# Kernel optimization log

Measured on AMD Instinct MI355X. Metric: run time of the kernel, lower is better.

Reference implementation:

```python
import jax, jax.numpy as jnp
import numpy as np

NUM_TEAMS = 100000
INPUT_SIZE = 128
HIDDEN = 128
NUM_MATCHES = 1000000
OUT = 3


def setup_inputs() -> dict:
    key = jax.random.key(0)
    ks = jax.random.split(key, 10)
    s_ih = 1.0 / np.sqrt(HIDDEN)
    inputs = jax.random.normal(ks[0], (NUM_TEAMS, INPUT_SIZE), dtype=jnp.float32)
    hx = jax.random.normal(ks[1], (NUM_TEAMS, HIDDEN), dtype=jnp.float32)
    cx = jax.random.normal(ks[2], (NUM_TEAMS, HIDDEN), dtype=jnp.float32)
    matches = jax.random.randint(ks[3], (NUM_MATCHES, 2), 0, NUM_TEAMS, dtype=jnp.int64)
    W_ih = jax.random.uniform(ks[4], (4 * HIDDEN, INPUT_SIZE), jnp.float32, -s_ih, s_ih)
    W_hh = jax.random.uniform(ks[5], (4 * HIDDEN, HIDDEN), jnp.float32, -s_ih, s_ih)
    b_ih = jax.random.uniform(ks[6], (4 * HIDDEN,), jnp.float32, -s_ih, s_ih)
    b_hh = jax.random.uniform(ks[7], (4 * HIDDEN,), jnp.float32, -s_ih, s_ih)
    s_o = 1.0 / np.sqrt(2 * HIDDEN)
    W_out = jax.random.uniform(ks[8], (OUT, 2 * HIDDEN), jnp.float32, -s_o, s_o)
    b_out = jax.random.uniform(ks[9], (OUT,), jnp.float32, -s_o, s_o)
    return {"inputs": inputs, "hx": hx, "cx": cx, "matches": matches,
            "W_ih": W_ih, "W_hh": W_hh, "b_ih": b_ih, "b_hh": b_hh,
            "W_out": W_out, "b_out": b_out}


def reference(inputs, hx, cx, matches, W_ih, W_hh, b_ih, b_hh, W_out, b_out):
    # Batched LSTMCell step across all teams (replaces per-team Python loop).
    gates = inputs @ W_ih.T + b_ih + hx @ W_hh.T + b_hh  # [T, 4H]
    i_g, f_g, g_g, o_g = jnp.split(gates, 4, axis=1)
    c_new = jax.nn.sigmoid(f_g) * cx + jax.nn.sigmoid(i_g) * jnp.tanh(g_g)
    h_new = jax.nn.sigmoid(o_g) * jnp.tanh(c_new)  # [T, H]
    # Fused gather + concat + linear + softmax for all matches.
    home = h_new[matches[:, 0]]  # [M, H]
    away = h_new[matches[:, 1]]  # [M, H]
    feat = jnp.concatenate([home, away], axis=1)  # [M, 2H]
    logits = feat @ W_out.T + b_out  # [M, 3]
    pmf = jax.nn.softmax(logits, axis=-1)
    return pmf
```

## Files before the change

### kernel.cpp

```cpp
#include <hip/hip_runtime.h>
#include <hip/hip_bf16.h>

typedef __bf16 bf16x8 __attribute__((ext_vector_type(8)));
typedef float f32x4 __attribute__((ext_vector_type(4)));

#define NUM_TEAMS 100000
#define NUM_MATCHES 1000000
#define LOG2E 1.4426950408889634f
#define NWG 3126
#define XQ 390
#define XR 6

__device__ __forceinline__ unsigned short f2bf(float x) {
    __hip_bfloat16 h = __float2bfloat16(x);
    return reinterpret_cast<unsigned short&>(h);
}
__device__ __forceinline__ unsigned int cvtpk(float a, float b) {
    unsigned int r;
    asm("v_cvt_pk_bf16_f32 %0, %1, %2" : "=v"(r) : "v"(a), "v"(b));
    return r;
}
__device__ __forceinline__ float exp2_(float x) {
    float r; asm("v_exp_f32 %0, %1" : "=v"(r) : "v"(x)); return r;
}
__device__ __forceinline__ float rcp_(float x) {
    float r; asm("v_rcp_f32 %0, %1" : "=v"(r) : "v"(x)); return r;
}

__global__ __launch_bounds__(256) void prep_kernel(
    const float* __restrict__ W_ih, const float* __restrict__ W_hh,
    const float* __restrict__ b_ih, const float* __restrict__ b_hh,
    unsigned short* __restrict__ Wpk, float* __restrict__ biasc)
{
    int gid = blockIdx.x * 256 + threadIdx.x;
    int e = gid & 7;
    int chunk = gid >> 3;
    int l15 = chunk & 15;
    int l4 = (chunk >> 4) & 3;
    int rest = chunk >> 6;
    int ks = rest & 7;
    int gate = (rest >> 3) & 3;
    int G = rest >> 5;
    int row = gate * 128 + G * 16 + l15;
    int k = ks * 32 + l4 * 8 + e;
    float v = (k < 128) ? W_ih[row * 128 + k] : W_hh[row * 128 + (k - 128)];
    Wpk[gid] = f2bf(v);
    if (gid < 512) {
        float b = b_ih[gid] + b_hh[gid];
        float scale = ((gid >> 7) == 2) ? (2.0f * LOG2E) : (-LOG2E);
        biasc[gid] = b * scale;
    }
}

__global__ __launch_bounds__(256, 4) void lstm_kernel(
    const float* __restrict__ inputs, const float* __restrict__ hx,
    const float* __restrict__ cx, const unsigned short* __restrict__ Wpk,
    const float* __restrict__ biasc, const float* __restrict__ W_out,
    float* __restrict__ projP)
{
    __shared__ __align__(16) unsigned short Abf[64 * 256];
    __shared__ float Wlds[768];
    const int tid = threadIdx.x;

    const int orig = blockIdx.x;
    const int xcd = orig & 7, idx = orig >> 3;
    const int wgid = (xcd < XR ? xcd * (XQ + 1) : XR * (XQ + 1) + (xcd - XR) * XQ) + idx;
    const int tile = wgid >> 1, ch = wgid & 1;
    const int brow = tile * 64;

    const int lane = tid & 63;
    const int w = tid >> 6;
    const int l15 = lane & 15, l4 = lane >> 4;
    const int hl = w * 16 + l15;
    const int hcol = ch * 64 + hl;

    {
        const int r0 = tid >> 4, seg = tid & 15;
        #pragma unroll
        for (int p = 0; p < 4; ++p) {
            int r = p * 16 + r0;
            int team = brow + r; if (team >= NUM_TEAMS) team = NUM_TEAMS - 1;
            const float* src = (seg < 8) ? inputs + (size_t)team * 128 + seg * 16
                                         : hx + (size_t)team * 128 + (seg - 8) * 16;
            float4 v0 = *reinterpret_cast<const float4*>(src);
            float4 v1 = *reinterpret_cast<const float4*>(src + 4);
            float4 v2 = *reinterpret_cast<const float4*>(src + 8);
            float4 v3 = *reinterpret_cast<const float4*>(src + 12);
            char* lbw = reinterpret_cast<char*>(Abf);
            int base = r * 512 + seg * 32;
            int swz = (r & 7) << 4;
            uint4 q0, q1;
            q0.x = cvtpk(v0.x, v0.y); q0.y = cvtpk(v0.z, v0.w);
            q0.z = cvtpk(v1.x, v1.y); q0.w = cvtpk(v1.z, v1.w);
            q1.x = cvtpk(v2.x, v2.y); q1.y = cvtpk(v2.z, v2.w);
            q1.z = cvtpk(v3.x, v3.y); q1.w = cvtpk(v3.z, v3.w);
            *reinterpret_cast<uint4*>(lbw + (base ^ swz)) = q0;
            *reinterpret_cast<uint4*>(lbw + ((base + 16) ^ swz)) = q1;
        }
        Wlds[tid] = W_out[tid];
        Wlds[256 + tid] = W_out[256 + tid];
        Wlds[512 + tid] = W_out[512 + tid];
    }

    const unsigned short* bpg = Wpk + (size_t)(ch * 4 + w) * 16384 + lane * 8;
    const float bic = biasc[hcol];
    const float bfc = biasc[128 + hcol];
    const float bgc = biasc[256 + hcol];
    const float boc = biasc[384 + hcol];
    const int swzA = (l15 & 7) << 4;
    const int kf = l4 * 16;
    const char* pArow = reinterpret_cast<const char*>(Abf) + l15 * 512;

    f32x4 acc[4][4] = {};

    __syncthreads();

    #pragma unroll
    for (int ks = 0; ks < 8; ++ks) {
        bf16x8 b0 = *(const bf16x8*)(bpg + ks * 512);
        bf16x8 b1 = *(const bf16x8*)(bpg + 4096 + ks * 512);
        bf16x8 b2 = *(const bf16x8*)(bpg + 8192 + ks * 512);
        bf16x8 b3 = *(const bf16x8*)(bpg + 12288 + ks * 512);
        const int ko = (ks * 64 + kf) ^ swzA;
        #pragma unroll
        for (int m = 0; m < 4; ++m) {
            bf16x8 af = *(const bf16x8*)(pArow + m * 8192 + ko);
            acc[m][0] = __builtin_amdgcn_mfma_f32_16x16x32_bf16(af, b0, acc[m][0], 0, 0, 0);
            acc[m][1] = __builtin_amdgcn_mfma_f32_16x16x32_bf16(af, b1, acc[m][1], 0, 0, 0);
            acc[m][2] = __builtin_amdgcn_mfma_f32_16x16x32_bf16(af, b2, acc[m][2], 0, 0, 0);
            acc[m][3] = __builtin_amdgcn_mfma_f32_16x16x32_bf16(af, b3, acc[m][3], 0, 0, 0);
        }
    }

    float cxa[16];
    #pragma unroll
    for (int m = 0; m < 4; ++m)
        #pragma unroll
        for (int j = 0; j < 4; ++j) {
            int team = brow + m * 16 + l4 * 4 + j;
            if (team >= NUM_TEAMS) team = NUM_TEAMS - 1;
            cxa[m * 4 + j] = cx[(size_t)team * 128 + hcol];
        }

    __syncthreads();

    {
        char* lb = reinterpret_cast<char*>(Abf);
        #pragma unroll
        for (int m = 0; m < 4; ++m) {
            #pragma unroll
            for (int j = 0; j < 4; ++j) {
                float si = rcp_(1.0f + exp2_(fmaf(acc[m][0][j], -LOG2E, bic)));
                float sf = rcp_(1.0f + exp2_(fmaf(acc[m][1][j], -LOG2E, bfc)));
                float tg = fmaf(-2.0f, rcp_(1.0f + exp2_(fmaf(acc[m][2][j], 2.0f * LOG2E, bgc))), 1.0f);
                float so = rcp_(1.0f + exp2_(fmaf(acc[m][3][j], -LOG2E, boc)));
                float cn = fmaf(sf, cxa[m * 4 + j], si * tg);
                float tc = fmaf(-2.0f, rcp_(1.0f + exp2_(cn * (2.0f * LOG2E))), 1.0f);
                float hn = so * tc;
                int t = m * 16 + l4 * 4 + j;
                *reinterpret_cast<float*>(lb + ((t * 256 + hl * 4) ^ ((t & 7) << 4))) = hn;
            }
        }
    }
    __syncthreads();

    {
        int tl = tid >> 2, sub = tid & 3;
        const char* lb = reinterpret_cast<const char*>(Abf);
        int hbase = tl * 256 + sub * 64;
        int hswz = (tl & 7) << 4;
        float a0 = 0.f, a1 = 0.f, a2 = 0.f, a3 = 0.f, a4 = 0.f, a5 = 0.f;
        #pragma unroll
        for (int c = 0; c < 4; ++c) {
            f32x4 h4 = *reinterpret_cast<const f32x4*>(lb + ((hbase + c * 16) ^ hswz));
            #pragma unroll
            for (int i = 0; i < 4; ++i) {
                float h = h4[i];
                int col = ch * 64 + sub * 16 + c * 4 + i;
                a0 += h * Wlds[col];       a1 += h * Wlds[256 + col]; a2 += h * Wlds[512 + col];
                a3 += h * Wlds[128 + col]; a4 += h * Wlds[384 + col]; a5 += h * Wlds[640 + col];
            }
        }
        a0 += __shfl_xor(a0, 1); a1 += __shfl_xor(a1, 1); a2 += __shfl_xor(a2, 1);
        a3 += __shfl_xor(a3, 1); a4 += __shfl_xor(a4, 1); a5 += __shfl_xor(a5, 1);
        a0 += __shfl_xor(a0, 2); a1 += __shfl_xor(a1, 2); a2 += __shfl_xor(a2, 2);
        a3 += __shfl_xor(a3, 2); a4 += __shfl_xor(a4, 2); a5 += __shfl_xor(a5, 2);
        int team = brow + tl;
        if (sub == 0 && team < NUM_TEAMS) {
            float4* o = reinterpret_cast<float4*>(projP + (size_t)team * 16 + ch * 8);
            o[0] = make_float4(a0, a1, a2, a2);
            o[1] = make_float4(a3, a4, a5, a5);
        }
    }
}

__global__ __launch_bounds__(256) void match_kernel(
    const int* __restrict__ matches, const float* __restrict__ projP,
    const float* __restrict__ b_out, float* __restrict__ out)
{
    int m = blockIdx.x * 256 + threadIdx.x;
    if (m >= NUM_MATCHES) return;
    int2 mi = reinterpret_cast<const int2*>(matches)[m];
    const float4* pp = reinterpret_cast<const float4*>(projP);
    float4 h0 = pp[(size_t)mi.x * 4 + 0];
    float4 h1 = pp[(size_t)mi.x * 4 + 2];
    float4 a0 = pp[(size_t)mi.y * 4 + 1];
    float4 a1 = pp[(size_t)mi.y * 4 + 3];
    float l0 = h0.x + h1.x + a0.x + a1.x + b_out[0];
    float l1 = h0.y + h1.y + a0.y + a1.y + b_out[1];
    float l2 = h0.z + h1.z + a0.z + a1.z + b_out[2];
    float mx = fmaxf(l0, fmaxf(l1, l2));
    float e0 = __expf(l0 - mx), e1 = __expf(l1 - mx), e2 = __expf(l2 - mx);
    float inv = 1.0f / (e0 + e1 + e2);
    out[3 * m + 0] = e0 * inv;
    out[3 * m + 1] = e1 * inv;
    out[3 * m + 2] = e2 * inv;
}

extern "C" void kernel_launch(void* const* d_in, const int* in_sizes, int n_in,
                              void* d_out, int out_size, void* d_ws, size_t ws_size,
                              hipStream_t stream) {
    const float* inputs = (const float*)d_in[0];
    const float* hx     = (const float*)d_in[1];
    const float* cx     = (const float*)d_in[2];
    const int*   matches= (const int*)d_in[3];
    const float* W_ih   = (const float*)d_in[4];
    const float* W_hh   = (const float*)d_in[5];
    const float* b_ih   = (const float*)d_in[6];
    const float* b_hh   = (const float*)d_in[7];
    const float* W_out  = (const float*)d_in[8];
    const float* b_out  = (const float*)d_in[9];
    float* out = (float*)d_out;

    char* ws = (char*)d_ws;
    unsigned short* Wpk  = (unsigned short*)ws;
    float* biasc         = (float*)(ws + 262144);
    float* projP         = (float*)(ws + (1 << 20));

    prep_kernel <<<512, 256, 0, stream>>>(W_ih, W_hh, b_ih, b_hh, Wpk, biasc);
    lstm_kernel <<<NWG, 256, 0, stream>>>(inputs, hx, cx, Wpk, biasc, W_out, projP);
    match_kernel<<<(NUM_MATCHES + 255) / 256, 256, 0, stream>>>(matches, projP, b_out, out);
}
```

Before: 77.26 us.

## Use one 512-thread block per team tile with direct global-to-LDS fp32 loads

Each workgroup now computes all 128 hidden columns for a 64-team tile with 8 waves, instead of splitting the columns across two workgroups. The A tile is loaded as fp32 straight into LDS via global_load_lds, and the bf16 conversion moves into the MFMA loop. The projection buffer shrinks to 8 floats per team, so match_kernel does two gathers per match instead of four. The cost is a doubled LDS footprint (64 KB fp32 tile), which lowers occupancy, plus extra conversion work repeated by every wave inside the inner loop.

```diff
diff --git a/kernel.cpp b/kernel.cpp
--- a/kernel.cpp
+++ b/kernel.cpp
@@ -7,9 +7,9 @@
 #define NUM_TEAMS 100000
 #define NUM_MATCHES 1000000
 #define LOG2E 1.4426950408889634f
-#define NWG 3126
-#define XQ 390
-#define XR 6
+#define NWG 1563
+#define XQ 195
+#define XR 3
 
 __device__ __forceinline__ unsigned short f2bf(float x) {
     __hip_bfloat16 h = __float2bfloat16(x);
@@ -25,6 +25,11 @@
 }
 __device__ __forceinline__ float rcp_(float x) {
     float r; asm("v_rcp_f32 %0, %1" : "=v"(r) : "v"(x)); return r;
+}
+__device__ __forceinline__ void load_lds16(const float* g, float* l) {
+    __builtin_amdgcn_global_load_lds(
+        (const __attribute__((address_space(1))) void*)g,
+        (__attribute__((address_space(3))) void*)l, 16, 0, 0);
 }
 
 __global__ __launch_bounds__(256) void prep_kernel(
@@ -52,79 +57,71 @@
     }
 }
 
-__global__ __launch_bounds__(256, 4) void lstm_kernel(
+__global__ __launch_bounds__(512, 4) void lstm_kernel(
     const float* __restrict__ inputs, const float* __restrict__ hx,
     const float* __restrict__ cx, const unsigned short* __restrict__ Wpk,
     const float* __restrict__ biasc, const float* __restrict__ W_out,
     float* __restrict__ projP)
 {
-    __shared__ __align__(16) unsigned short Abf[64 * 256];
+    __shared__ __align__(16) float Af[64 * 256];
     __shared__ float Wlds[768];
     const int tid = threadIdx.x;
 
     const int orig = blockIdx.x;
     const int xcd = orig & 7, idx = orig >> 3;
-    const int wgid = (xcd < XR ? xcd * (XQ + 1) : XR * (XQ + 1) + (xcd - XR) * XQ) + idx;
-    const int tile = wgid >> 1, ch = wgid & 1;
+    const int tile = (xcd < XR ? xcd * (XQ + 1) : XR * (XQ + 1) + (xcd - XR) * XQ) + idx;
     const int brow = tile * 64;
 
     const int lane = tid & 63;
     const int w = tid >> 6;
     const int l15 = lane & 15, l4 = lane >> 4;
-    const int hl = w * 16 + l15;
-    const int hcol = ch * 64 + hl;
+    const int hcol = w * 16 + l15;
 
     {
-        const int r0 = tid >> 4, seg = tid & 15;
-        #pragma unroll
-        for (int p = 0; p < 4; ++p) {
-            int r = p * 16 + r0;
-            int team = brow + r; if (team >= NUM_TEAMS) team = NUM_TEAMS - 1;
-            const float* src = (seg < 8) ? inputs + (size_t)team * 128 + seg * 16
-                                         : hx + (size_t)team * 128 + (seg - 8) * 16;
-            float4 v0 = *reinterpret_cast<const float4*>(src);
-            float4 v1 = *reinterpret_cast<const float4*>(src + 4);
-            float4 v2 = *reinterpret_cast<const float4*>(src + 8);
-            float4 v3 = *reinterpret_cast<const float4*>(src + 12);
-            char* lbw = reinterpret_cast<char*>(Abf);
-            int base = r * 512 + seg * 32;
-            int swz = (r & 7) << 4;
-            uint4 q0, q1;
-            q0.x = cvtpk(v0.x, v0.y); q0.y = cvtpk(v0.z, v0.w);
-            q0.z = cvtpk(v1.x, v1.y); q0.w = cvtpk(v1.z, v1.w);
-            q1.x = cvtpk(v2.x, v2.y); q1.y = cvtpk(v2.z, v2.w);
-            q1.z = cvtpk(v3.x, v3.y); q1.w = cvtpk(v3.z, v3.w);
-            *reinterpret_cast<uint4*>(lbw + (base ^ swz)) = q0;
-            *reinterpret_cast<uint4*>(lbw + ((base + 16) ^ swz)) = q1;
+        const int su = lane ^ w;
+        const int col = su * 4;
+        const float* base = (col < 128) ? inputs + col : hx + (col - 128);
+        #pragma unroll
+        for (int p = 0; p < 8; ++p) {
+            int row = p * 8 + w;
+            int team = brow + row; if (team >= NUM_TEAMS) team = NUM_TEAMS - 1;
+            load_lds16(base + (size_t)team * 128, Af + row * 256 + lane * 4);
         }
         Wlds[tid] = W_out[tid];
-        Wlds[256 + tid] = W_out[256 + tid];
-        Wlds[512 + tid] = W_out[512 + tid];
-    }
-
-    const unsigned short* bpg = Wpk + (size_t)(ch * 4 + w) * 16384 + lane * 8;
+        if (tid < 256) Wlds[512 + tid] = W_out[512 + tid];
+    }
+
+    const unsigned short* bpg = Wpk + (size_t)w * 16384 + lane * 8;
     const float bic = biasc[hcol];
     const float bfc = biasc[128 + hcol];
     const float bgc = biasc[256 + hcol];
     const float boc = biasc[384 + hcol];
-    const int swzA = (l15 & 7) << 4;
-    const int kf = l4 * 16;
-    const char* pArow = reinterpret_cast<const char*>(Abf) + l15 * 512;
+    const int u0 = ((l4 * 2) ^ (l15 & 7)) << 4;
+    const int u1 = ((l4 * 2 + 1) ^ (l15 & 7)) << 4;
 
     f32x4 acc[4][4] = {};
 
+    asm volatile("s_waitcnt vmcnt(0)" ::: "memory");
     __syncthreads();
 
+    const char* Ab = reinterpret_cast<const char*>(Af);
     #pragma unroll
     for (int ks = 0; ks < 8; ++ks) {
         bf16x8 b0 = *(const bf16x8*)(bpg + ks * 512);
         bf16x8 b1 = *(const bf16x8*)(bpg + 4096 + ks * 512);
         bf16x8 b2 = *(const bf16x8*)(bpg + 8192 + ks * 512);
         bf16x8 b3 = *(const bf16x8*)(bpg + 12288 + ks * 512);
-        const int ko = (ks * 64 + kf) ^ swzA;
         #pragma unroll
         for (int m = 0; m < 4; ++m) {
-            bf16x8 af = *(const bf16x8*)(pArow + m * 8192 + ko);
+            const char* pa = Ab + (m * 16 + l15) * 1024 + ks * 128;
+            f32x4 a0 = *reinterpret_cast<const f32x4*>(pa + u0);
+            f32x4 a1 = *reinterpret_cast<const f32x4*>(pa + u1);
+            union { uint4 q; bf16x8 v; } cc;
+            cc.q.x = cvtpk(a0[0], a0[1]);
+            cc.q.y = cvtpk(a0[2], a0[3]);
+            cc.q.z = cvtpk(a1[0], a1[1]);
+            cc.q.w = cvtpk(a1[2], a1[3]);
+            bf16x8 af = cc.v;
             acc[m][0] = __builtin_amdgcn_mfma_f32_16x16x32_bf16(af, b0, acc[m][0], 0, 0, 0);
             acc[m][1] = __builtin_amdgcn_mfma_f32_16x16x32_bf16(af, b1, acc[m][1], 0, 0, 0);
             acc[m][2] = __builtin_amdgcn_mfma_f32_16x16x32_bf16(af, b2, acc[m][2], 0, 0, 0);
@@ -145,7 +142,7 @@
     __syncthreads();
 
     {
-        char* lb = reinterpret_cast<char*>(Abf);
+        char* lb = reinterpret_cast<char*>(Af);
         #pragma unroll
         for (int m = 0; m < 4; ++m) {
             #pragma unroll
@@ -158,16 +155,16 @@
                 float tc = fmaf(-2.0f, rcp_(1.0f + exp2_(cn * (2.0f * LOG2E))), 1.0f);
                 float hn = so * tc;
                 int t = m * 16 + l4 * 4 + j;
-                *reinterpret_cast<float*>(lb + ((t * 256 + hl * 4) ^ ((t & 7) << 4))) = hn;
+                *reinterpret_cast<float*>(lb + ((t * 512 + hcol * 4) ^ ((t & 7) << 4))) = hn;
             }
         }
     }
     __syncthreads();
 
     {
-        int tl = tid >> 2, sub = tid & 3;
-        const char* lb = reinterpret_cast<const char*>(Abf);
-        int hbase = tl * 256 + sub * 64;
+        int tl = tid >> 3, sub = tid & 7;
+        const char* lb = reinterpret_cast<const char*>(Af);
+        int hbase = tl * 512 + sub * 64;
         int hswz = (tl & 7) << 4;
         float a0 = 0.f, a1 = 0.f, a2 = 0.f, a3 = 0.f, a4 = 0.f, a5 = 0.f;
         #pragma unroll
@@ -176,7 +173,7 @@
             #pragma unroll
             for (int i = 0; i < 4; ++i) {
                 float h = h4[i];
-                int col = ch * 64 + sub * 16 + c * 4 + i;
+                int col = sub * 16 + c * 4 + i;
                 a0 += h * Wlds[col];       a1 += h * Wlds[256 + col]; a2 += h * Wlds[512 + col];
                 a3 += h * Wlds[128 + col]; a4 += h * Wlds[384 + col]; a5 += h * Wlds[640 + col];
             }
@@ -185,9 +182,11 @@
         a3 += __shfl_xor(a3, 1); a4 += __shfl_xor(a4, 1); a5 += __shfl_xor(a5, 1);
         a0 += __shfl_xor(a0, 2); a1 += __shfl_xor(a1, 2); a2 += __shfl_xor(a2, 2);
         a3 += __shfl_xor(a3, 2); a4 += __shfl_xor(a4, 2); a5 += __shfl_xor(a5, 2);
+        a0 += __shfl_xor(a0, 4); a1 += __shfl_xor(a1, 4); a2 += __shfl_xor(a2, 4);
+        a3 += __shfl_xor(a3, 4); a4 += __shfl_xor(a4, 4); a5 += __shfl_xor(a5, 4);
         int team = brow + tl;
         if (sub == 0 && team < NUM_TEAMS) {
-            float4* o = reinterpret_cast<float4*>(projP + (size_t)team * 16 + ch * 8);
+            float4* o = reinterpret_cast<float4*>(projP + (size_t)team * 8);
             o[0] = make_float4(a0, a1, a2, a2);
             o[1] = make_float4(a3, a4, a5, a5);
         }
@@ -202,13 +201,11 @@
     if (m >= NUM_MATCHES) return;
     int2 mi = reinterpret_cast<const int2*>(matches)[m];
     const float4* pp = reinterpret_cast<const float4*>(projP);
-    float4 h0 = pp[(size_t)mi.x * 4 + 0];
-    float4 h1 = pp[(size_t)mi.x * 4 + 2];
-    float4 a0 = pp[(size_t)mi.y * 4 + 1];
-    float4 a1 = pp[(size_t)mi.y * 4 + 3];
-    float l0 = h0.x + h1.x + a0.x + a1.x + b_out[0];
-    float l1 = h0.y + h1.y + a0.y + a1.y + b_out[1];
-    float l2 = h0.z + h1.z + a0.z + a1.z + b_out[2];
+    float4 hv = pp[(size_t)mi.x * 2 + 0];
+    float4 av = pp[(size_t)mi.y * 2 + 1];
+    float l0 = hv.x + av.x + b_out[0];
+    float l1 = hv.y + av.y + b_out[1];
+    float l2 = hv.z + av.z + b_out[2];
     float mx = fmaxf(l0, fmaxf(l1, l2));
     float e0 = __expf(l0 - mx), e1 = __expf(l1 - mx), e2 = __expf(l2 - mx);
     float inv = 1.0f / (e0 + e1 + e2);
@@ -238,6 +235,6 @@
     float* projP         = (float*)(ws + (1 << 20));
 
     prep_kernel <<<512, 256, 0, stream>>>(W_ih, W_hh, b_ih, b_hh, Wpk, biasc);
-    lstm_kernel <<<NWG, 256, 0, stream>>>(inputs, hx, cx, Wpk, biasc, W_out, projP);
+    lstm_kernel <<<NWG, 512, 0, stream>>>(inputs, hx, cx, Wpk, biasc, W_out, projP);
     match_kernel<<<(NUM_MATCHES + 255) / 256, 256, 0, stream>>>(matches, projP, b_out, out);
 }
```

Measured after the change: 80.34 us. 4.0% more time.

## Prefetch cx tile into LDS via async global_load_lds and batch input loads

Applied to the files above, without the earlier changes.

The cx tile is now fetched at kernel start with direct global-to-LDS async loads, replacing the strided per-element scalar global loads that happened after the GEMM loop. The input/hx staging loop is split so all 16 float4 loads are issued before any conversion, which increases memory-level parallelism. The added 16 KB LDS buffer and higher register use force the launch bound down to 3 waves per SIMD, trading occupancy for better latency hiding.

```diff
diff --git a/kernel.cpp b/kernel.cpp
--- a/kernel.cpp
+++ b/kernel.cpp
@@ -25,6 +25,11 @@
 }
 __device__ __forceinline__ float rcp_(float x) {
     float r; asm("v_rcp_f32 %0, %1" : "=v"(r) : "v"(x)); return r;
+}
+__device__ __forceinline__ void load_lds16(const float* g, float* l) {
+    __builtin_amdgcn_global_load_lds(
+        (const __attribute__((address_space(1))) void*)g,
+        (__attribute__((address_space(3))) void*)l, 16, 0, 0);
 }
 
 __global__ __launch_bounds__(256) void prep_kernel(
@@ -52,13 +57,14 @@
     }
 }
 
-__global__ __launch_bounds__(256, 4) void lstm_kernel(
+__global__ __launch_bounds__(256, 3) void lstm_kernel(
     const float* __restrict__ inputs, const float* __restrict__ hx,
     const float* __restrict__ cx, const unsigned short* __restrict__ Wpk,
     const float* __restrict__ biasc, const float* __restrict__ W_out,
     float* __restrict__ projP)
 {
     __shared__ __align__(16) unsigned short Abf[64 * 256];
+    __shared__ __align__(16) float cxl[64 * 64];
     __shared__ float Wlds[768];
     const int tid = threadIdx.x;
 
@@ -75,25 +81,38 @@
     const int hcol = ch * 64 + hl;
 
     {
+        #pragma unroll
+        for (int p = 0; p < 4; ++p) {
+            int r = (p * 4 + w) * 4 + l4;
+            int team = brow + r; if (team >= NUM_TEAMS) team = NUM_TEAMS - 1;
+            load_lds16(cx + (size_t)team * 128 + ch * 64 + l15 * 4,
+                       cxl + (p * 4 + w) * 256 + lane * 4);
+        }
+    }
+
+    {
         const int r0 = tid >> 4, seg = tid & 15;
+        const float* srcb = (seg < 8) ? inputs + seg * 16 : hx + (seg - 8) * 16;
+        float4 v[16];
         #pragma unroll
         for (int p = 0; p < 4; ++p) {
-            int r = p * 16 + r0;
-            int team = brow + r; if (team >= NUM_TEAMS) team = NUM_TEAMS - 1;
-            const float* src = (seg < 8) ? inputs + (size_t)team * 128 + seg * 16
-                                         : hx + (size_t)team * 128 + (seg - 8) * 16;
-            float4 v0 = *reinterpret_cast<const float4*>(src);
-            float4 v1 = *reinterpret_cast<const float4*>(src + 4);
-            float4 v2 = *reinterpret_cast<const float4*>(src + 8);
-            float4 v3 = *reinterpret_cast<const float4*>(src + 12);
-            char* lbw = reinterpret_cast<char*>(Abf);
-            int base = r * 512 + seg * 32;
-            int swz = (r & 7) << 4;
+            int team = brow + p * 16 + r0; if (team >= NUM_TEAMS) team = NUM_TEAMS - 1;
+            const float* src = srcb + (size_t)team * 128;
+            v[p * 4 + 0] = *reinterpret_cast<const float4*>(src);
+            v[p * 4 + 1] = *reinterpret_cast<const float4*>(src + 4);
+            v[p * 4 + 2] = *reinterpret_cast<const float4*>(src + 8);
+            v[p * 4 + 3] = *reinterpret_cast<const float4*>(src + 12);
+        }
+        char* lbw = reinterpret_cast<char*>(Abf);
+        const int swz = (r0 & 7) << 4;
+        #pragma unroll
+        for (int p = 0; p < 4; ++p) {
+            int base = (p * 16 + r0) * 512 + seg * 32;
             uint4 q0, q1;
-            q0.x = cvtpk(v0.x, v0.y); q0.y = cvtpk(v0.z, v0.w);
-            q0.z = cvtpk(v1.x, v1.y); q0.w = cvtpk(v1.z, v1.w);
-            q1.x = cvtpk(v2.x, v2.y); q1.y = cvtpk(v2.z, v2.w);
-            q1.z = cvtpk(v3.x, v3.y); q1.w = cvtpk(v3.z, v3.w);
+            q0.x = cvtpk(v[p*4+0].x, v[p*4+0].y); q0.y = cvtpk(v[p*4+0].z, v[p*4+0].w);
+            q0.z = cvtpk(v[p*4+1].x, v[p*4+1].y); q0.w = cvtpk(v[p*4+1].z, v[p*4+1].w);
+            q1.x = cvtpk(v[p*4+2].x, v[p*4+2].y); q1.y = cvtpk(v[p*4+2].z, v[p*4+2].w);
+            q1.z = cvtpk(v[p*4+3].x, v[p*4+3].y); q1.w = cvtpk(v[p*4+3].z, v[p*4+3].w);
             *reinterpret_cast<uint4*>(lbw + (base ^ swz)) = q0;
             *reinterpret_cast<uint4*>(lbw + ((base + 16) ^ swz)) = q1;
         }
@@ -132,16 +151,6 @@
         }
     }
 
-    float cxa[16];
-    #pragma unroll
-    for (int m = 0; m < 4; ++m)
-        #pragma unroll
-        for (int j = 0; j < 4; ++j) {
-            int team = brow + m * 16 + l4 * 4 + j;
-            if (team >= NUM_TEAMS) team = NUM_TEAMS - 1;
-            cxa[m * 4 + j] = cx[(size_t)team * 128 + hcol];
-        }
-
     __syncthreads();
 
     {
@@ -150,11 +159,12 @@
         for (int m = 0; m < 4; ++m) {
             #pragma unroll
             for (int j = 0; j < 4; ++j) {
+                float cxv = cxl[(m * 16 + l4 * 4 + j) * 64 + hl];
                 float si = rcp_(1.0f + exp2_(fmaf(acc[m][0][j], -LOG2E, bic)));
                 float sf = rcp_(1.0f + exp2_(fmaf(acc[m][1][j], -LOG2E, bfc)));
                 float tg = fmaf(-2.0f, rcp_(1.0f + exp2_(fmaf(acc[m][2][j], 2.0f * LOG2E, bgc))), 1.0f);
                 float so = rcp_(1.0f + exp2_(fmaf(acc[m][3][j], -LOG2E, boc)));
-                float cn = fmaf(sf, cxa[m * 4 + j], si * tg);
+                float cn = fmaf(sf, cxv, si * tg);
                 float tc = fmaf(-2.0f, rcp_(1.0f + exp2_(cn * (2.0f * LOG2E))), 1.0f);
                 float hn = so * tc;
                 int t = m * 16 + l4 * 4 + j;
```

Result: slower. 79.56 us (+3.0%).

## Halve LSTM tile to 32 teams, stage cx via async LDS loads

Applied to the files above, without the earlier changes.

Shrinks each workgroup's team tile from 64 to 32 rows, which doubles the grid and lets the launch bound allow five workgroups per CU. cx is now prefetched straight into LDS with global_load_lds at kernel start instead of being gathered into registers after the MFMA loop, so that load overlaps with the compute. Bounds clamping is dropped because 100000 divides evenly by 32. The trade-off is that each workgroup reloads the packed weights while doing half the work, so weight traffic per team doubles.

```diff
diff --git a/kernel.cpp b/kernel.cpp
--- a/kernel.cpp
+++ b/kernel.cpp
@@ -7,9 +7,9 @@
 #define NUM_TEAMS 100000
 #define NUM_MATCHES 1000000
 #define LOG2E 1.4426950408889634f
-#define NWG 3126
-#define XQ 390
-#define XR 6
+#define NWG 6250
+#define XQ 781
+#define XR 2
 
 __device__ __forceinline__ unsigned short f2bf(float x) {
     __hip_bfloat16 h = __float2bfloat16(x);
@@ -25,6 +25,11 @@
 }
 __device__ __forceinline__ float rcp_(float x) {
     float r; asm("v_rcp_f32 %0, %1" : "=v"(r) : "v"(x)); return r;
+}
+__device__ __forceinline__ void load_lds16(const float* g, float* l) {
+    __builtin_amdgcn_global_load_lds(
+        (const __attribute__((address_space(1))) void*)g,
+        (__attribute__((address_space(3))) void*)l, 16, 0, 0);
 }
 
 __global__ __launch_bounds__(256) void prep_kernel(
@@ -52,13 +57,14 @@
     }
 }
 
-__global__ __launch_bounds__(256, 4) void lstm_kernel(
+__global__ __launch_bounds__(256, 5) void lstm_kernel(
     const float* __restrict__ inputs, const float* __restrict__ hx,
     const float* __restrict__ cx, const unsigned short* __restrict__ Wpk,
     const float* __restrict__ biasc, const float* __restrict__ W_out,
     float* __restrict__ projP)
 {
-    __shared__ __align__(16) unsigned short Abf[64 * 256];
+    __shared__ __align__(16) unsigned short Abf[32 * 256];
+    __shared__ __align__(16) float cxl[8 * 260];
     __shared__ float Wlds[768];
     const int tid = threadIdx.x;
 
@@ -66,7 +72,7 @@
     const int xcd = orig & 7, idx = orig >> 3;
     const int wgid = (xcd < XR ? xcd * (XQ + 1) : XR * (XQ + 1) + (xcd - XR) * XQ) + idx;
     const int tile = wgid >> 1, ch = wgid & 1;
-    const int brow = tile * 64;
+    const int brow = tile * 32;
 
     const int lane = tid & 63;
     const int w = tid >> 6;
@@ -75,20 +81,28 @@
     const int hcol = ch * 64 + hl;
 
     {
+        #pragma unroll
+        for (int p = 0; p < 2; ++p) {
+            int team = brow + p * 16 + w * 4 + l4;
+            load_lds16(cx + (size_t)team * 128 + ch * 64 + l15 * 4,
+                       cxl + (p * 4 + w) * 260 + lane * 4);
+        }
+    }
+
+    {
         const int r0 = tid >> 4, seg = tid & 15;
-        #pragma unroll
-        for (int p = 0; p < 4; ++p) {
+        const float* srcb = (seg < 8) ? inputs + seg * 16 : hx + (seg - 8) * 16;
+        char* lbw = reinterpret_cast<char*>(Abf);
+        const int swz = (r0 & 7) << 4;
+        #pragma unroll
+        for (int p = 0; p < 2; ++p) {
             int r = p * 16 + r0;
-            int team = brow + r; if (team >= NUM_TEAMS) team = NUM_TEAMS - 1;
-            const float* src = (seg < 8) ? inputs + (size_t)team * 128 + seg * 16
-                                         : hx + (size_t)team * 128 + (seg - 8) * 16;
+            const float* src = srcb + (size_t)(brow + r) * 128;
             float4 v0 = *reinterpret_cast<const float4*>(src);
             float4 v1 = *reinterpret_cast<const float4*>(src + 4);
             float4 v2 = *reinterpret_cast<const float4*>(src + 8);
             float4 v3 = *reinterpret_cast<const float4*>(src + 12);
-            char* lbw = reinterpret_cast<char*>(Abf);
             int base = r * 512 + seg * 32;
-            int swz = (r & 7) << 4;
             uint4 q0, q1;
             q0.x = cvtpk(v0.x, v0.y); q0.y = cvtpk(v0.z, v0.w);
             q0.z = cvtpk(v1.x, v1.y); q0.w = cvtpk(v1.z, v1.w);
@@ -111,7 +125,7 @@
     const int kf = l4 * 16;
     const char* pArow = reinterpret_cast<const char*>(Abf) + l15 * 512;
 
-    f32x4 acc[4][4] = {};
+    f32x4 acc[2][4] = {};
 
     __syncthreads();
 
@@ -123,7 +137,7 @@
         bf16x8 b3 = *(const bf16x8*)(bpg + 12288 + ks * 512);
         const int ko = (ks * 64 + kf) ^ swzA;
         #pragma unroll
-        for (int m = 0; m < 4; ++m) {
+        for (int m = 0; m < 2; ++m) {
             bf16x8 af = *(const bf16x8*)(pArow + m * 8192 + ko);
             acc[m][0] = __builtin_amdgcn_mfma_f32_16x16x32_bf16(af, b0, acc[m][0], 0, 0, 0);
             acc[m][1] = __builtin_amdgcn_mfma_f32_16x16x32_bf16(af, b1, acc[m][1], 0, 0, 0);
@@ -132,29 +146,20 @@
         }
     }
 
-    float cxa[16];
-    #pragma unroll
-    for (int m = 0; m < 4; ++m)
-        #pragma unroll
-        for (int j = 0; j < 4; ++j) {
-            int team = brow + m * 16 + l4 * 4 + j;
-            if (team >= NUM_TEAMS) team = NUM_TEAMS - 1;
-            cxa[m * 4 + j] = cx[(size_t)team * 128 + hcol];
-        }
-
     __syncthreads();
 
     {
         char* lb = reinterpret_cast<char*>(Abf);
         #pragma unroll
-        for (int m = 0; m < 4; ++m) {
+        for (int m = 0; m < 2; ++m) {
             #pragma unroll
             for (int j = 0; j < 4; ++j) {
+                float cxv = cxl[(m * 4 + l4) * 260 + j * 64 + hl];
                 float si = rcp_(1.0f + exp2_(fmaf(acc[m][0][j], -LOG2E, bic)));
                 float sf = rcp_(1.0f + exp2_(fmaf(acc[m][1][j], -LOG2E, bfc)));
                 float tg = fmaf(-2.0f, rcp_(1.0f + exp2_(fmaf(acc[m][2][j], 2.0f * LOG2E, bgc))), 1.0f);
                 float so = rcp_(1.0f + exp2_(fmaf(acc[m][3][j], -LOG2E, boc)));
-                float cn = fmaf(sf, cxa[m * 4 + j], si * tg);
+                float cn = fmaf(sf, cxv, si * tg);
                 float tc = fmaf(-2.0f, rcp_(1.0f + exp2_(cn * (2.0f * LOG2E))), 1.0f);
                 float hn = so * tc;
                 int t = m * 16 + l4 * 4 + j;
@@ -165,18 +170,18 @@
     __syncthreads();
 
     {
-        int tl = tid >> 2, sub = tid & 3;
+        int tl = tid >> 3, sub = tid & 7;
         const char* lb = reinterpret_cast<const char*>(Abf);
-        int hbase = tl * 256 + sub * 64;
+        int hbase = tl * 256 + sub * 32;
         int hswz = (tl & 7) << 4;
         float a0 = 0.f, a1 = 0.f, a2 = 0.f, a3 = 0.f, a4 = 0.f, a5 = 0.f;
         #pragma unroll
-        for (int c = 0; c < 4; ++c) {
+        for (int c = 0; c < 2; ++c) {
             f32x4 h4 = *reinterpret_cast<const f32x4*>(lb + ((hbase + c * 16) ^ hswz));
             #pragma unroll
             for (int i = 0; i < 4; ++i) {
                 float h = h4[i];
-                int col = ch * 64 + sub * 16 + c * 4 + i;
+                int col = ch * 64 + sub * 8 + c * 4 + i;
                 a0 += h * Wlds[col];       a1 += h * Wlds[256 + col]; a2 += h * Wlds[512 + col];
                 a3 += h * Wlds[128 + col]; a4 += h * Wlds[384 + col]; a5 += h * Wlds[640 + col];
             }
@@ -185,8 +190,10 @@
         a3 += __shfl_xor(a3, 1); a4 += __shfl_xor(a4, 1); a5 += __shfl_xor(a5, 1);
         a0 += __shfl_xor(a0, 2); a1 += __shfl_xor(a1, 2); a2 += __shfl_xor(a2, 2);
         a3 += __shfl_xor(a3, 2); a4 += __shfl_xor(a4, 2); a5 += __shfl_xor(a5, 2);
+        a0 += __shfl_xor(a0, 4); a1 += __shfl_xor(a1, 4); a2 += __shfl_xor(a2, 4);
+        a3 += __shfl_xor(a3, 4); a4 += __shfl_xor(a4, 4); a5 += __shfl_xor(a5, 4);
         int team = brow + tl;
-        if (sub == 0 && team < NUM_TEAMS) {
+        if (sub == 0) {
             float4* o = reinterpret_cast<float4*>(projP + (size_t)team * 16 + ch * 8);
             o[0] = make_float4(a0, a1, a2, a2);
             o[1] = make_float4(a3, a4, a5, a5);
```

New measurement: 82.12 us. +6.3%, slower.
